# Kernel optimization log

Hardware: AMD Instinct MI355X
Metric: run time of the kernel (lower is better)

Reference implementation:

```python
import jax, jax.numpy as jnp
import numpy as np

N_NODES = 100000


def sage_conv(x, edge_index, Wl, Wr, b):
    # PyG SAGEConv(aggr='mean'): out = lin_l(mean_{j in N(i)} x_j) + lin_r(x_i)
    src, dst = edge_index[0], edge_index[1]
    msg = x[src]                                    # [E, d] gather
    agg = jax.ops.segment_sum(msg, dst, num_segments=N_NODES)
    cnt = jax.ops.segment_sum(jnp.ones((src.shape[0],), dtype=x.dtype), dst,
                              num_segments=N_NODES)
    mean = agg / jnp.maximum(cnt, 1.0)[:, None]     # isolated nodes -> 0
    return mean @ Wl + x @ Wr + b


def setup_inputs() -> dict:
    key = jax.random.key(0)
    ks = jax.random.split(key, 7)
    N, E, d_in, d_hid, d_out = N_NODES, 1000000, 64, 128, 64
    x = jax.random.normal(ks[0], (N, d_in), dtype=jnp.float32)
    W1l = jax.random.normal(ks[1], (d_in, d_hid), dtype=jnp.float32) / np.sqrt(d_in)
    W1r = jax.random.normal(ks[2], (d_in, d_hid), dtype=jnp.float32) / np.sqrt(d_in)
    b1 = jnp.zeros((d_hid,), dtype=jnp.float32)
    W2l = jax.random.normal(ks[3], (d_hid, d_out), dtype=jnp.float32) / np.sqrt(d_hid)
    W2r = jax.random.normal(ks[4], (d_hid, d_out), dtype=jnp.float32) / np.sqrt(d_hid)
    b2 = jnp.zeros((d_out,), dtype=jnp.float32)
    edge_index = jax.random.randint(ks[5], (2, E), 0, N, dtype=jnp.int64)
    return {"x": x, "W1l": W1l, "W1r": W1r, "b1": b1,
            "W2l": W2l, "W2r": W2r, "b2": b2, "edge_index": edge_index}


def reference(x, W1l, W1r, b1, W2l, W2r, b2, edge_index):
    h = jax.nn.relu(sage_conv(x, edge_index, W1l, W1r, b1))
    out = sage_conv(h, edge_index, W2l, W2r, b2)
    return out
```

## Files before the change

kernel.cpp:

```cpp
#include <hip/hip_runtime.h>

#define N_NODES 100000
#define N_EDGES 1000000
#define DEG_CAP 64
#define OVF_CAP 4096
#define SPILL_CAP 4096

#define BKT_SH 8
#define BKT_NODES 256
#define NBKT 392
#define BKT_CAP 4096
#define BIN_CHUNK 4096
#define FIFO_CAP 32

typedef __attribute__((ext_vector_type(8))) short bf16x8;
typedef __attribute__((ext_vector_type(4))) float f32x4;

__device__ __forceinline__ unsigned short f2bf(float f) {
    unsigned u = __float_as_uint(f);
    return (unsigned short)((u + 0x7FFF + ((u >> 16) & 1)) >> 16);
}
__device__ __forceinline__ float bf2f(unsigned short b) {
    return __uint_as_float(((unsigned)b) << 16);
}
__device__ __forceinline__ float bflo(unsigned u) {
    return __uint_as_float(u << 16);
}
__device__ __forceinline__ float bfhi(unsigned u) {
    return __uint_as_float(u & 0xffff0000u);
}
__device__ __forceinline__ void split_rbf(float f, unsigned short& ho,
                                          unsigned short& lo) {
    unsigned short hb = f2bf(f);
    ho = hb;
    lo = f2bf(f - bf2f(hb));
}


__global__ __launch_bounds__(256) void prep_kernel(
        const float4* __restrict__ x4,
        ushort4* __restrict__ xh4, ushort4* __restrict__ xl4,
        const float* __restrict__ W1l, const float* __restrict__ W1r,
        const float* __restrict__ W2l, const float* __restrict__ W2r,
        short* __restrict__ Bf1, short* __restrict__ Bf2,
        int4* __restrict__ gcur4, int* __restrict__ ovfc,
        int* __restrict__ spillc) {
    int i = blockIdx.x * blockDim.x + threadIdx.x;
    if (i < 128) gcur4[i] = make_int4(0, 0, 0, 0);
    if (i == 0) { *ovfc = 0; *spillc = 0; }
    if (i < 32768) {
        int g = i >> 14;
        int e = i & 16383;
        int k = e >> 7;
        int n = e & 127;
        float v;
        if (g == 0) v = (k < 64) ? W1l[k * 128 + n] : W1r[(k - 64) * 128 + n];
        else        v = (n < 64) ? W2l[k * 64 + n]  : W2r[k * 64 + (n - 64)];
        unsigned short hb, lb;
        split_rbf(v, hb, lb);
        int c = n >> 4, kc = k >> 5;
        int lane = (((k >> 3) & 3) << 4) | (n & 15);
        int j = k & 7;
        short* base = g ? Bf2 : Bf1;
        base[((c * 4 + kc) * 2 + 0) * 512 + lane * 8 + j] = (short)hb;
        base[((c * 4 + kc) * 2 + 1) * 512 + lane * 8 + j] = (short)lb;
    }
    if (i < N_NODES * 16) {
        float4 v = x4[i];
        ushort4 oh, ol;
        split_rbf(v.x, oh.x, ol.x);
        split_rbf(v.y, oh.y, ol.y);
        split_rbf(v.z, oh.z, ol.z);
        split_rbf(v.w, oh.w, ol.w);
        xh4[i] = oh;
        xl4[i] = ol;
    }
}

__global__ __launch_bounds__(256) void bin_kernel(
        const int* __restrict__ ei, unsigned* __restrict__ rec,
        int* __restrict__ gcur, int* __restrict__ spillc,
        int2* __restrict__ spill) {
    __shared__ int lcnt[NBKT];
    __shared__ unsigned fifo[NBKT * FIFO_CAP];
    for (int i = threadIdx.x; i < NBKT; i += 256) lcnt[i] = 0;
    __syncthreads();
    int base = blockIdx.x * BIN_CHUNK;
    int end = base + BIN_CHUNK;
    if (end > N_EDGES) end = N_EDGES;
    for (int e = base + threadIdx.x; e < end; e += 256) {
        int s = ei[e];
        int d = ei[N_EDGES + e];
        int b = d >> BKT_SH;
        unsigned r = ((unsigned)s << BKT_SH) | (unsigned)(d & (BKT_NODES - 1));
        int pos = atomicAdd(&lcnt[b], 1);
        if (pos < FIFO_CAP) {
            fifo[b * FIFO_CAP + pos] = r;
        } else {
            int o = atomicAdd(spillc, 1);
            if (o < SPILL_CAP) spill[o] = make_int2(s, d);
        }
    }
    __syncthreads();
    for (int b = threadIdx.x; b < NBKT; b += 256) {
        int cnt = lcnt[b];
        if (cnt > FIFO_CAP) cnt = FIFO_CAP;
        if (cnt == 0) continue;
        int gb = atomicAdd(&gcur[b], cnt);
        for (int k = 0; k < cnt; ++k) {
            int g = gb + k;
            unsigned r = fifo[b * FIFO_CAP + k];
            if (g < BKT_CAP) {
                rec[b * BKT_CAP + g] = r;
            } else {
                int o = atomicAdd(spillc, 1);
                if (o < SPILL_CAP)
                    spill[o] = make_int2((int)(r >> BKT_SH),
                                         (b << BKT_SH) | (int)(r & (BKT_NODES - 1)));
            }
        }
    }
}

__global__ __launch_bounds__(256) void build_kernel(
        const unsigned* __restrict__ rec, const int* __restrict__ gcur,
        int* __restrict__ counts, int* __restrict__ slots,
        int* __restrict__ ovfc, int* __restrict__ ovf) {
    __shared__ int lcnt[BKT_NODES];
    __shared__ int lslots[BKT_NODES * DEG_CAP];
    int b = blockIdx.x;
    for (int i = threadIdx.x; i < BKT_NODES; i += 256) lcnt[i] = 0;
    __syncthreads();
    int n = gcur[b];
    if (n > BKT_CAP) n = BKT_CAP;
    for (int i = threadIdx.x; i < n; i += 256) {
        unsigned r = rec[b * BKT_CAP + i];
        int dlo = (int)(r & (BKT_NODES - 1));
        int src = (int)(r >> BKT_SH);
        int pos = atomicAdd(&lcnt[dlo], 1);
        if (pos < DEG_CAP) {
            lslots[dlo * DEG_CAP + pos] = src;
        } else {
            int o = atomicAdd(ovfc, 1);
            if (o < OVF_CAP) {
                ovf[o * 2] = src;
                ovf[o * 2 + 1] = (b << BKT_SH) | dlo;
            }
        }
    }
    __syncthreads();
    int nodeBase = b << BKT_SH;
    for (int i = threadIdx.x; i < BKT_NODES; i += 256)
        counts[nodeBase + i] = lcnt[i];
    const int4* ls4 = (const int4*)lslots;
    int4* gs4 = (int4*)(slots + nodeBase * DEG_CAP);
    for (int i = threadIdx.x; i < BKT_NODES * DEG_CAP / 4; i += 256)
        gs4[i] = ls4[i];
}

__global__ __launch_bounds__(64) void spill_fix_kernel(
        const int2* __restrict__ spill, const int* __restrict__ spillc,
        int* __restrict__ counts, int* __restrict__ slots,
        int* __restrict__ ovfc, int* __restrict__ ovf) {
    int n = *spillc;
    if (n > SPILL_CAP) n = SPILL_CAP;
    int i = blockIdx.x * 64 + threadIdx.x;
    if (i >= n) return;
    int s = spill[i].x;
    int d = spill[i].y;
    int pos = atomicAdd(&counts[d], 1);
    if (pos < DEG_CAP) {
        slots[d * DEG_CAP + pos] = s;
    } else {
        int o = atomicAdd(ovfc, 1);
        if (o < OVF_CAP) { ovf[o * 2] = s; ovf[o * 2 + 1] = d; }
    }
}

__global__ __launch_bounds__(256) void gather_bf_kernel(
        const unsigned short* __restrict__ feat, const int* __restrict__ counts,
        const int* __restrict__ slots,
        unsigned short* __restrict__ mh, unsigned short* __restrict__ ml) {
    int wid = blockIdx.x * 4 + (threadIdx.x >> 6);
    int l = threadIdx.x & 63;
    if (wid >= N_NODES) return;
    int deg = counts[wid];
    int dcap = min(deg, DEG_CAP);
    int ids = slots[wid * DEG_CAP + l];
    const int grp = l >> 4;
    const int fb = (l & 15) * 4;
    float s0 = 0.f, s1 = 0.f, s2 = 0.f, s3 = 0.f;
    int j = 0;
    for (; j + 8 <= dcap; j += 8) {
        int sA = __shfl(ids, j + grp);
        int sB = __shfl(ids, j + 4 + grp);
        uint2 uA = *(const uint2*)(feat + sA * 64 + fb);
        uint2 uB = *(const uint2*)(feat + sB * 64 + fb);
        s0 += bflo(uA.x) + bflo(uB.x);
        s1 += bfhi(uA.x) + bfhi(uB.x);
        s2 += bflo(uA.y) + bflo(uB.y);
        s3 += bfhi(uA.y) + bfhi(uB.y);
    }
    for (; j < dcap; j += 4) {
        int nb = j + grp;
        bool v = nb < dcap;
        int s = __shfl(ids, v ? nb : 0);
        uint2 u = *(const uint2*)(feat + s * 64 + fb);
        if (v) {
            s0 += bflo(u.x);
            s1 += bfhi(u.x);
            s2 += bflo(u.y);
            s3 += bfhi(u.y);
        }
    }
    s0 += __shfl_xor(s0, 16); s0 += __shfl_xor(s0, 32);
    s1 += __shfl_xor(s1, 16); s1 += __shfl_xor(s1, 32);
    s2 += __shfl_xor(s2, 16); s2 += __shfl_xor(s2, 32);
    s3 += __shfl_xor(s3, 16); s3 += __shfl_xor(s3, 32);
    if (l < 16) {
        float inv = 1.0f / fmaxf((float)deg, 1.0f);
        ushort4 oh, ol;
        split_rbf(s0 * inv, oh.x, ol.x);
        split_rbf(s1 * inv, oh.y, ol.y);
        split_rbf(s2 * inv, oh.z, ol.z);
        split_rbf(s3 * inv, oh.w, ol.w);
        *(ushort4*)&mh[wid * 64 + fb] = oh;
        *(ushort4*)&ml[wid * 64 + fb] = ol;
    }
}

__global__ __launch_bounds__(64) void ovf_mean_fix_kernel(
        const float* __restrict__ x, const int* __restrict__ ovf,
        const int* __restrict__ ovfc, const int* __restrict__ counts,
        unsigned short* __restrict__ mh, unsigned short* __restrict__ ml) {
    int n = *ovfc;
    if (n > OVF_CAP) n = OVF_CAP;
    int t = threadIdx.x;
    for (int idx = 0; idx < n; ++idx) {
        int s = ovf[idx * 2];
        int d = ovf[idx * 2 + 1];
        float inv = 1.0f / fmaxf((float)counts[d], 1.0f);
        float m = bf2f(mh[d * 64 + t]) + bf2f(ml[d * 64 + t])
                + x[s * 64 + t] * inv;
        unsigned short hb, lb;
        split_rbf(m, hb, lb);
        mh[d * 64 + t] = hb;
        ml[d * 64 + t] = lb;
        __syncthreads();
    }
}

__global__ __launch_bounds__(256) void mlp_fused_kernel(
        const unsigned short* __restrict__ mh, const unsigned short* __restrict__ ml,
        const unsigned short* __restrict__ xh, const unsigned short* __restrict__ xl,
        const short* __restrict__ Bf1, const float* __restrict__ b1,
        const short* __restrict__ Bf2, const float* __restrict__ b2,
        unsigned short* __restrict__ p_bf, float* __restrict__ q) {
    __shared__ unsigned short h_lds[128][136];
    const int w = threadIdx.x >> 6;
    const int l = threadIdx.x & 63;
    const int lane15 = l & 15;
    const int quad = l >> 4;
    const int rowBase = blockIdx.x * 128;

    {
        bf16x8 bh[2][4], bl[2][4];
#pragma unroll
        for (int ci = 0; ci < 2; ++ci) {
            const int c = 2 * w + ci;
#pragma unroll
            for (int kc = 0; kc < 4; ++kc) {
                const short* bp = Bf1 + ((c * 4 + kc) * 2) * 512 + l * 8;
                bh[ci][kc] = *(const bf16x8*)bp;
                bl[ci][kc] = *(const bf16x8*)(bp + 512);
            }
        }
        float bias[2];
#pragma unroll
        for (int ci = 0; ci < 2; ++ci) bias[ci] = b1[(2 * w + ci) * 16 + lane15];

#pragma unroll
        for (int rt = 0; rt < 8; ++rt) {
            const int row = rowBase + rt * 16 + lane15;
            const bool rv = row < N_NODES;
            const bf16x8 zz = {0, 0, 0, 0, 0, 0, 0, 0};

            bf16x8 ah[4], al[4];
#pragma unroll
            for (int kc = 0; kc < 4; ++kc) {
                if (rv) {
                    const int off = (kc < 2)
                        ? row * 64 + kc * 32 + quad * 8
                        : row * 64 + (kc - 2) * 32 + quad * 8;
                    const unsigned short* ph = (kc < 2) ? (mh + off) : (xh + off);
                    const unsigned short* pl = (kc < 2) ? (ml + off) : (xl + off);
                    ah[kc] = *(const bf16x8*)ph;
                    al[kc] = *(const bf16x8*)pl;
                } else {
                    ah[kc] = zz;
                    al[kc] = zz;
                }
            }

            f32x4 acc[2] = {(f32x4){0.f, 0.f, 0.f, 0.f}, (f32x4){0.f, 0.f, 0.f, 0.f}};
#pragma unroll
            for (int kc = 0; kc < 4; ++kc) {
#pragma unroll
                for (int ci = 0; ci < 2; ++ci) {
                    acc[ci] = __builtin_amdgcn_mfma_f32_16x16x32_bf16(ah[kc], bh[ci][kc], acc[ci], 0, 0, 0);
                    acc[ci] = __builtin_amdgcn_mfma_f32_16x16x32_bf16(al[kc], bh[ci][kc], acc[ci], 0, 0, 0);
                    acc[ci] = __builtin_amdgcn_mfma_f32_16x16x32_bf16(ah[kc], bl[ci][kc], acc[ci], 0, 0, 0);
                }
            }

            const int rloc = rt * 16 + quad * 4;
#pragma unroll
            for (int ci = 0; ci < 2; ++ci) {
                const int col = (2 * w + ci) * 16 + lane15;
#pragma unroll
                for (int i = 0; i < 4; ++i)
                    h_lds[rloc + i][col] =
                        f2bf(fmaxf(acc[ci][i] + bias[ci], 0.f));
            }
        }
    }
    __syncthreads();

    {
        bf16x8 bh[2][4], bl[2][4];
#pragma unroll
        for (int ci = 0; ci < 2; ++ci) {
            const int c = 2 * w + ci;
#pragma unroll
            for (int kc = 0; kc < 4; ++kc) {
                const short* bp = Bf2 + ((c * 4 + kc) * 2) * 512 + l * 8;
                bh[ci][kc] = *(const bf16x8*)bp;
                bl[ci][kc] = *(const bf16x8*)(bp + 512);
            }
        }
        float bias[2];
#pragma unroll
        for (int ci = 0; ci < 2; ++ci) {
            const int c = 2 * w + ci;
            bias[ci] = (c >= 4) ? b2[(c - 4) * 16 + lane15] : 0.f;
        }

#pragma unroll
        for (int rt = 0; rt < 8; ++rt) {
            bf16x8 ah[4];
#pragma unroll
            for (int kc = 0; kc < 4; ++kc)
                ah[kc] = *(const bf16x8*)&h_lds[rt * 16 + lane15][kc * 32 + quad * 8];

            f32x4 acc[2] = {(f32x4){0.f, 0.f, 0.f, 0.f}, (f32x4){0.f, 0.f, 0.f, 0.f}};
#pragma unroll
            for (int kc = 0; kc < 4; ++kc) {
#pragma unroll
                for (int ci = 0; ci < 2; ++ci) {
                    acc[ci] = __builtin_amdgcn_mfma_f32_16x16x32_bf16(ah[kc], bh[ci][kc], acc[ci], 0, 0, 0);
                    acc[ci] = __builtin_amdgcn_mfma_f32_16x16x32_bf16(ah[kc], bl[ci][kc], acc[ci], 0, 0, 0);
                }
            }

            const int rb = rowBase + rt * 16 + quad * 4;
#pragma unroll
            for (int ci = 0; ci < 2; ++ci) {
                const int c = 2 * w + ci;
                if (c < 4) {
#pragma unroll
                    for (int i = 0; i < 4; ++i) {
                        int r = rb + i;
                        if (r < N_NODES)
                            p_bf[r * 64 + c * 16 + lane15] = f2bf(acc[ci][i]);
                    }
                } else {
#pragma unroll
                    for (int i = 0; i < 4; ++i) {
                        int r = rb + i;
                        if (r < N_NODES)
                            q[r * 64 + (c - 4) * 16 + lane15] = acc[ci][i] + bias[ci];
                    }
                }
            }
        }
    }
}

__global__ __launch_bounds__(256) void gather_final_kernel(
        const unsigned short* __restrict__ p, const int* __restrict__ counts,
        const int* __restrict__ slots, const float* __restrict__ q,
        float* __restrict__ out) {
    int wid = blockIdx.x * 4 + (threadIdx.x >> 6);
    int l = threadIdx.x & 63;
    if (wid >= N_NODES) return;
    int deg = counts[wid];
    int dcap = min(deg, DEG_CAP);
    int ids = slots[wid * DEG_CAP + l];
    const int grp = l >> 4;
    const int fb = (l & 15) * 4;
    float s0 = 0.f, s1 = 0.f, s2 = 0.f, s3 = 0.f;
    int j = 0;
    for (; j + 8 <= dcap; j += 8) {
        int sA = __shfl(ids, j + grp);
        int sB = __shfl(ids, j + 4 + grp);
        uint2 uA = *(const uint2*)(p + sA * 64 + fb);
        uint2 uB = *(const uint2*)(p + sB * 64 + fb);
        s0 += bflo(uA.x) + bflo(uB.x);
        s1 += bfhi(uA.x) + bfhi(uB.x);
        s2 += bflo(uA.y) + bflo(uB.y);
        s3 += bfhi(uA.y) + bfhi(uB.y);
    }
    for (; j < dcap; j += 4) {
        int nb = j + grp;
        bool v = nb < dcap;
        int s = __shfl(ids, v ? nb : 0);
        uint2 u = *(const uint2*)(p + s * 64 + fb);
        if (v) {
            s0 += bflo(u.x);
            s1 += bfhi(u.x);
            s2 += bflo(u.y);
            s3 += bfhi(u.y);
        }
    }
    s0 += __shfl_xor(s0, 16); s0 += __shfl_xor(s0, 32);
    s1 += __shfl_xor(s1, 16); s1 += __shfl_xor(s1, 32);
    s2 += __shfl_xor(s2, 16); s2 += __shfl_xor(s2, 32);
    s3 += __shfl_xor(s3, 16); s3 += __shfl_xor(s3, 32);
    if (l < 16) {
        float inv = 1.0f / fmaxf((float)deg, 1.0f);
        float4 qv = *(const float4*)&q[wid * 64 + fb];
        *(float4*)&out[wid * 64 + fb] =
            make_float4(s0 * inv + qv.x, s1 * inv + qv.y,
                        s2 * inv + qv.z, s3 * inv + qv.w);
    }
}

__global__ __launch_bounds__(64) void ovf_fixup_kernel(
        const unsigned short* __restrict__ p, const int* __restrict__ ovf,
        const int* __restrict__ ovfc, const int* __restrict__ counts,
        float* __restrict__ out) {
    int n = *ovfc;
    if (n > OVF_CAP) n = OVF_CAP;
    for (int idx = blockIdx.x; idx < n; idx += gridDim.x) {
        int s = ovf[idx * 2];
        int d = ovf[idx * 2 + 1];
        float inv = 1.0f / fmaxf((float)counts[d], 1.0f);
        atomicAdd(&out[d * 64 + threadIdx.x],
                  bf2f(p[s * 64 + threadIdx.x]) * inv);
    }
}

extern "C" void kernel_launch(void* const* d_in, const int* in_sizes, int n_in,
                              void* d_out, int out_size, void* d_ws, size_t ws_size,
                              hipStream_t stream) {
    const float* x   = (const float*)d_in[0];
    const float* W1l = (const float*)d_in[1];
    const float* W1r = (const float*)d_in[2];
    const float* b1  = (const float*)d_in[3];
    const float* W2l = (const float*)d_in[4];
    const float* W2r = (const float*)d_in[5];
    const float* b2  = (const float*)d_in[6];
    const int*   ei  = (const int*)d_in[7];

    int*   wsi      = (int*)d_ws;
    float* wsf      = (float*)d_ws;
    int*   counts   = wsi;
    int*   ovfc     = wsi + 100352;
    int*   spillc   = wsi + 100353;
    int*   gcur     = wsi + 100416;
    int*   ovf      = wsi + 100928;
    int2*  spill    = (int2*)(wsi + 109120);
    short* Bf1      = (short*)(wsi + 117312);
    short* Bf2      = (short*)(wsi + 133696);
    int*   slots    = wsi + 150080;
    unsigned* rec   = (unsigned*)(wsi + 6572608);
    unsigned short* xh = (unsigned short*)(wsi + 8178240);
    unsigned short* xl = (unsigned short*)(wsi + 11378240);
    unsigned short* mh = (unsigned short*)(wsi + 14578240);
    unsigned short* ml = (unsigned short*)(wsi + 17778240);
    unsigned short* p_bf = (unsigned short*)(wsi + 20978240);
    float* q        = wsf + 24178240;
    float* out      = (float*)d_out;

    prep_kernel<<<(N_NODES * 16 + 255) / 256, 256, 0, stream>>>(
        (const float4*)x, (ushort4*)xh, (ushort4*)xl, W1l, W1r, W2l, W2r,
        Bf1, Bf2, (int4*)gcur, ovfc, spillc);

    bin_kernel<<<(N_EDGES + BIN_CHUNK - 1) / BIN_CHUNK, 256, 0, stream>>>(
        ei, rec, gcur, spillc, spill);
    build_kernel<<<NBKT, 256, 0, stream>>>(rec, gcur, counts, slots, ovfc, ovf);
    spill_fix_kernel<<<SPILL_CAP / 64, 64, 0, stream>>>(
        spill, spillc, counts, slots, ovfc, ovf);

    gather_bf_kernel<<<(N_NODES + 3) / 4, 256, 0, stream>>>(
        xh, counts, slots, mh, ml);
    ovf_mean_fix_kernel<<<1, 64, 0, stream>>>(x, ovf, ovfc, counts, mh, ml);

    mlp_fused_kernel<<<(N_NODES + 127) / 128, 256, 0, stream>>>(
        mh, ml, xh, xl, Bf1, b1, Bf2, b2, p_bf, q);

    gather_final_kernel<<<(N_NODES + 3) / 4, 256, 0, stream>>>(
        p_bf, counts, slots, q, out);
    ovf_fixup_kernel<<<64, 64, 0, stream>>>(p_bf, ovf, ovfc, counts, out);
}
```

Baseline: 229.3 us.

## Fold spill and overflow fixup kernels into build, MLP and gather kernels

```diff
diff --git a/kernel.cpp b/kernel.cpp
--- a/kernel.cpp
+++ b/kernel.cpp
@@ -124,6 +124,7 @@
 
 __global__ __launch_bounds__(256) void build_kernel(
         const unsigned* __restrict__ rec, const int* __restrict__ gcur,
+        const int2* __restrict__ spill, const int* __restrict__ spillc,
         int* __restrict__ counts, int* __restrict__ slots,
         int* __restrict__ ovfc, int* __restrict__ ovf) {
     __shared__ int lcnt[BKT_NODES];
@@ -148,6 +149,21 @@
             }
         }
     }
+    int ns = *spillc;
+    if (ns > SPILL_CAP) ns = SPILL_CAP;
+    for (int i = threadIdx.x; i < ns; i += 256) {
+        int2 e = spill[i];
+        if ((e.y >> BKT_SH) == b) {
+            int dlo = e.y & (BKT_NODES - 1);
+            int pos = atomicAdd(&lcnt[dlo], 1);
+            if (pos < DEG_CAP) {
+                lslots[dlo * DEG_CAP + pos] = e.x;
+            } else {
+                int o = atomicAdd(ovfc, 1);
+                if (o < OVF_CAP) { ovf[o * 2] = e.x; ovf[o * 2 + 1] = e.y; }
+            }
+        }
+    }
     __syncthreads();
     int nodeBase = b << BKT_SH;
     for (int i = threadIdx.x; i < BKT_NODES; i += 256)
@@ -156,25 +172,6 @@
     int4* gs4 = (int4*)(slots + nodeBase * DEG_CAP);
     for (int i = threadIdx.x; i < BKT_NODES * DEG_CAP / 4; i += 256)
         gs4[i] = ls4[i];
-}
-
-__global__ __launch_bounds__(64) void spill_fix_kernel(
-        const int2* __restrict__ spill, const int* __restrict__ spillc,
-        int* __restrict__ counts, int* __restrict__ slots,
-        int* __restrict__ ovfc, int* __restrict__ ovf) {
-    int n = *spillc;
-    if (n > SPILL_CAP) n = SPILL_CAP;
-    int i = blockIdx.x * 64 + threadIdx.x;
-    if (i >= n) return;
-    int s = spill[i].x;
-    int d = spill[i].y;
-    int pos = atomicAdd(&counts[d], 1);
-    if (pos < DEG_CAP) {
-        slots[d * DEG_CAP + pos] = s;
-    } else {
-        int o = atomicAdd(ovfc, 1);
-        if (o < OVF_CAP) { ovf[o * 2] = s; ovf[o * 2 + 1] = d; }
-    }
 }
 
 __global__ __launch_bounds__(256) void gather_bf_kernel(
@@ -229,39 +226,46 @@
     }
 }
 
-__global__ __launch_bounds__(64) void ovf_mean_fix_kernel(
-        const float* __restrict__ x, const int* __restrict__ ovf,
-        const int* __restrict__ ovfc, const int* __restrict__ counts,
-        unsigned short* __restrict__ mh, unsigned short* __restrict__ ml) {
-    int n = *ovfc;
-    if (n > OVF_CAP) n = OVF_CAP;
-    int t = threadIdx.x;
-    for (int idx = 0; idx < n; ++idx) {
-        int s = ovf[idx * 2];
-        int d = ovf[idx * 2 + 1];
-        float inv = 1.0f / fmaxf((float)counts[d], 1.0f);
-        float m = bf2f(mh[d * 64 + t]) + bf2f(ml[d * 64 + t])
-                + x[s * 64 + t] * inv;
-        unsigned short hb, lb;
-        split_rbf(m, hb, lb);
-        mh[d * 64 + t] = hb;
-        ml[d * 64 + t] = lb;
-        __syncthreads();
-    }
-}
-
 __global__ __launch_bounds__(256) void mlp_fused_kernel(
         const unsigned short* __restrict__ mh, const unsigned short* __restrict__ ml,
         const unsigned short* __restrict__ xh, const unsigned short* __restrict__ xl,
+        const float* __restrict__ x,
         const short* __restrict__ Bf1, const float* __restrict__ b1,
         const short* __restrict__ Bf2, const float* __restrict__ b2,
-        unsigned short* __restrict__ p_bf, float* __restrict__ q) {
+        const int* __restrict__ ovf, const int* __restrict__ ovfc,
+        const int* __restrict__ counts,
+        unsigned short* __restrict__ p_bf_out, float* __restrict__ q) {
     __shared__ unsigned short h_lds[128][136];
     const int w = threadIdx.x >> 6;
     const int l = threadIdx.x & 63;
     const int lane15 = l & 15;
     const int quad = l >> 4;
     const int rowBase = blockIdx.x * 128;
+
+    {
+        int n = *ovfc;
+        if (n > OVF_CAP) n = OVF_CAP;
+        if (n > 0) {
+            for (int idx = 0; idx < n; ++idx) {
+                int d = ovf[idx * 2 + 1];
+                if (d >= rowBase && d < rowBase + 128) {
+                    if (threadIdx.x < 64) {
+                        int s = ovf[idx * 2];
+                        int t = threadIdx.x;
+                        float inv = 1.0f / fmaxf((float)counts[d], 1.0f);
+                        float m = bf2f(mh[d * 64 + t]) + bf2f(ml[d * 64 + t])
+                                + x[s * 64 + t] * inv;
+                        unsigned short hb, lb;
+                        split_rbf(m, hb, lb);
+                        ((unsigned short*)mh)[d * 64 + t] = hb;
+                        ((unsigned short*)ml)[d * 64 + t] = lb;
+                    }
+                    __syncthreads();
+                }
+            }
+            __syncthreads();
+        }
+    }
 
     {
         bf16x8 bh[2][4], bl[2][4];
@@ -371,7 +375,7 @@
                     for (int i = 0; i < 4; ++i) {
                         int r = rb + i;
                         if (r < N_NODES)
-                            p_bf[r * 64 + c * 16 + lane15] = f2bf(acc[ci][i]);
+                            p_bf_out[r * 64 + c * 16 + lane15] = f2bf(acc[ci][i]);
                     }
                 } else {
 #pragma unroll
@@ -389,6 +393,7 @@
 __global__ __launch_bounds__(256) void gather_final_kernel(
         const unsigned short* __restrict__ p, const int* __restrict__ counts,
         const int* __restrict__ slots, const float* __restrict__ q,
+        const int* __restrict__ ovf, const int* __restrict__ ovfc,
         float* __restrict__ out) {
     int wid = blockIdx.x * 4 + (threadIdx.x >> 6);
     int l = threadIdx.x & 63;
@@ -427,26 +432,23 @@
     s2 += __shfl_xor(s2, 16); s2 += __shfl_xor(s2, 32);
     s3 += __shfl_xor(s3, 16); s3 += __shfl_xor(s3, 32);
     if (l < 16) {
+        int n = *ovfc;
+        if (n > OVF_CAP) n = OVF_CAP;
+        for (int idx = 0; idx < n; ++idx) {
+            if (ovf[idx * 2 + 1] == wid) {
+                int s = ovf[idx * 2];
+                uint2 u = *(const uint2*)(p + s * 64 + fb);
+                s0 += bflo(u.x);
+                s1 += bfhi(u.x);
+                s2 += bflo(u.y);
+                s3 += bfhi(u.y);
+            }
+        }
         float inv = 1.0f / fmaxf((float)deg, 1.0f);
         float4 qv = *(const float4*)&q[wid * 64 + fb];
         *(float4*)&out[wid * 64 + fb] =
             make_float4(s0 * inv + qv.x, s1 * inv + qv.y,
                         s2 * inv + qv.z, s3 * inv + qv.w);
-    }
-}
-
-__global__ __launch_bounds__(64) void ovf_fixup_kernel(
-        const unsigned short* __restrict__ p, const int* __restrict__ ovf,
-        const int* __restrict__ ovfc, const int* __restrict__ counts,
-        float* __restrict__ out) {
-    int n = *ovfc;
-    if (n > OVF_CAP) n = OVF_CAP;
-    for (int idx = blockIdx.x; idx < n; idx += gridDim.x) {
-        int s = ovf[idx * 2];
-        int d = ovf[idx * 2 + 1];
-        float inv = 1.0f / fmaxf((float)counts[d], 1.0f);
-        atomicAdd(&out[d * 64 + threadIdx.x],
-                  bf2f(p[s * 64 + threadIdx.x]) * inv);
     }
 }
 
@@ -488,18 +490,15 @@
 
     bin_kernel<<<(N_EDGES + BIN_CHUNK - 1) / BIN_CHUNK, 256, 0, stream>>>(
         ei, rec, gcur, spillc, spill);
-    build_kernel<<<NBKT, 256, 0, stream>>>(rec, gcur, counts, slots, ovfc, ovf);
-    spill_fix_kernel<<<SPILL_CAP / 64, 64, 0, stream>>>(
-        spill, spillc, counts, slots, ovfc, ovf);
+    build_kernel<<<NBKT, 256, 0, stream>>>(
+        rec, gcur, spill, spillc, counts, slots, ovfc, ovf);
 
     gather_bf_kernel<<<(N_NODES + 3) / 4, 256, 0, stream>>>(
         xh, counts, slots, mh, ml);
-    ovf_mean_fix_kernel<<<1, 64, 0, stream>>>(x, ovf, ovfc, counts, mh, ml);
 
     mlp_fused_kernel<<<(N_NODES + 127) / 128, 256, 0, stream>>>(
-        mh, ml, xh, xl, Bf1, b1, Bf2, b2, p_bf, q);
+        mh, ml, xh, xl, x, Bf1, b1, Bf2, b2, ovf, ovfc, counts, p_bf, q);
 
     gather_final_kernel<<<(N_NODES + 3) / 4, 256, 0, stream>>>(
-        p_bf, counts, slots, q, out);
-    ovf_fixup_kernel<<<64, 64, 0, stream>>>(p_bf, ovf, ovfc, counts, out);
-}
+        p_bf, counts, slots, q, ovf, ovfc, out);
+}
```

After: 228.5 us. Within noise of the previous version (-0.4%).
